# Performance work log

Measured on AMD Instinct MI355X. Metric: run time of the kernel, lower is better.

The kernel has to match this reference:

```python
import jax, jax.numpy as jnp
import numpy as np

B = 2048; S = 256; D = 64; R = 16; H = 4; HD = D // H; HID = 128; P = 4; T = 8
SCALE = 10.0  # pointer-address sharpness from _execute_read


def setup_inputs() -> dict:
    key = jax.random.key(0)
    ks = jax.random.split(key, 16)
    g = lambda k, shape, s=0.05: jax.random.normal(k, shape, dtype=jnp.float32) * s
    z = lambda shape: jnp.zeros(shape, jnp.float32)
    return {
        'x': g(ks[0], (B, D), 1.0),
        'register_init': g(ks[1], (R, D)),
        'scratchpad_init': g(ks[2], (S, D)),
        'pointer_init': z((P,)),
        'wq': g(ks[3], (D, D)), 'bq': z((D,)),
        'wk': g(ks[4], (D, D)), 'bk': z((D,)),
        'wv': g(ks[5], (D, D)), 'bv': z((D,)),
        'wo': g(ks[6], (D, D)), 'bo': z((D,)),
        'w_write': g(ks[7], (D, D)), 'b_write': z((D,)),
        'a_w1': g(ks[8], (D, HID)), 'a_b1': z((HID,)),
        'a_w2': g(ks[9], (HID, S)), 'a_b2': z((S,)),
        'p_w1': g(ks[10], (D, HID)), 'p_b1': z((HID,)),
        'p_w2': g(ks[11], (HID, D)), 'p_b2': z((D,)),
        'num_steps': T,
    }


def _engine_forward(x, register_init, scratchpad_init, pointer_init,
                    wq, bq, wk, bk, wv, bv, wo, bo, w_write, b_write,
                    a_w1, a_b1, a_w2, a_b2, p_w1, p_b1, p_w2, p_b2, num_steps):
    b = x.shape[0]
    positions = jnp.linspace(0.0, 1.0, S)  # (S,) slot positions for pointer addressing
    sp = jnp.broadcast_to(scratchpad_init, (b, S, D))
    reg = jnp.broadcast_to(register_init, (b, R, D))
    reg = reg.at[:, 0, :].set(x)  # LOAD: place input into register 0
    ptr = jnp.broadcast_to(pointer_init, (b, P))
    inv_sqrt = 1.0 / jnp.sqrt(jnp.float32(HD))

    def step(carry, _):
        sp, reg, ptr = carry
        # READ: soft pointer-based address over scratchpad slots (softmax(-|pos-p|*10))
        p0 = ptr[:, 0]                                                            # (b,)
        addr_r = jax.nn.softmax(-jnp.abs(positions[None, :] - p0[:, None]) * SCALE, axis=-1)  # (b,S)
        reg_val = jnp.einsum('bs,bsd->bd', addr_r, sp)                            # (b,D)
        reg = reg.at[:, 0, :].set(reg_val)
        # content-based attention read (read_head: 4-head MHA, q from register 0)
        qh = (reg_val @ wq + bq).reshape(b, H, HD)
        kh = (sp @ wk + bk).reshape(b, S, H, HD)
        vh = (sp @ wv + bv).reshape(b, S, H, HD)
        attn = jax.nn.softmax(jnp.einsum('bhd,bshd->bhs', qh, kh) * inv_sqrt, axis=-1)  # (b,H,S)
        read = jnp.einsum('bhs,bshd->bhd', attn, vh).reshape(b, D) @ wo + bo      # (b,D)
        # pattern_net transforms the read value into register 1
        patt = jax.nn.relu(read @ p_w1 + p_b1) @ p_w2 + p_b2
        reg = reg.at[:, 1, :].set(patt)
        # WRITE: address_net softmax write + write_head, gated blend into scratchpad
        addr_w = jax.nn.softmax(jax.nn.relu(read @ a_w1 + a_b1) @ a_w2 + a_b2, axis=-1)  # (b,S)
        wval = read @ w_write + b_write                                           # (b,D)
        aw = addr_w[:, :, None]
        sp = sp * (1.0 - aw) + wval[:, None, :] * aw
        # POINTER_MOVE: +1 slot (normalized), clamped to [0,1]
        ptr = ptr.at[:, 0].set(jnp.clip(p0 + 1.0 / S, 0.0, 1.0))
        return (sp, reg, ptr), None

    (sp, reg, ptr), _ = jax.lax.scan(step, (sp, reg, ptr), None, length=num_steps)
    return sp


def reference(x, register_init, scratchpad_init, pointer_init,
              wq, bq, wk, bk, wv, bv, wo, bo, w_write, b_write,
              a_w1, a_b1, a_w2, a_b2, p_w1, p_b1, p_w2, p_b2, num_steps):
    return _engine_forward(x, register_init, scratchpad_init, pointer_init,
                           wq, bq, wk, bk, wv, bv, wo, bo, w_write, b_write,
                           a_w1, a_b1, a_w2, a_b2, p_w1, p_b1, p_w2, p_b2, num_steps)
```

## Files before the change

### kernel.cpp

```cpp
#include <hip/hip_runtime.h>

#define NB   2048
#define S    256
#define D    64
#define H    4
#define HD   16
#define HID  128
#define TPB  256
#define SCALEF 10.0f

__device__ __forceinline__ float wred_max(float v){
#pragma unroll
  for (int m = 32; m >= 1; m >>= 1) v = fmaxf(v, __shfl_xor(v, m, 64));
  return v;
}
__device__ __forceinline__ float wred_sum(float v){
#pragma unroll
  for (int m = 32; m >= 1; m >>= 1) v += __shfl_xor(v, m, 64);
  return v;
}
__device__ __forceinline__ float pick4(float4 f, int h){
  float r = f.x;
  r = (h == 1) ? f.y : r;
  r = (h == 2) ? f.z : r;
  r = (h == 3) ? f.w : r;
  return r;
}

__global__ __launch_bounds__(TPB, 2)
void engine_kernel(const float* __restrict__ sp_init,
                   const float* __restrict__ ptr_init,
                   const float* __restrict__ wq, const float* __restrict__ bq,
                   const float* __restrict__ wk, const float* __restrict__ bk,
                   const float* __restrict__ wv, const float* __restrict__ bv,
                   const float* __restrict__ wo, const float* __restrict__ bo,
                   const float* __restrict__ ww, const float* __restrict__ bw,
                   const float* __restrict__ aw1, const float* __restrict__ ab1,
                   const float* __restrict__ aw2, const float* __restrict__ ab2,
                   const int*   __restrict__ nsteps,
                   float* __restrict__ out)
{
  __shared__ float  sp[S][D + 1];
  __shared__ float4 attnT[S];
  __shared__ float  addrv[S];
  __shared__ float4 qkT[D];
  __shared__ __align__(16) float hidden[HID];
  __shared__ float  parth[4][4][D];
  __shared__ float  regv[D], qhv[D], readf[D], readv[D], wvalv[D];
  __shared__ float  ctxv[H][D];
  __shared__ float  qbv[H];
  __shared__ float  red[8];

  const int tid  = threadIdx.x;
  const int wid  = tid >> 6;
  const int lane = tid & 63;

  float awcol[HID];
#pragma unroll
  for (int k = 0; k < HID; ++k) awcol[k] = aw2[k * S + tid];

  for (int i = tid; i < S * D / 4; i += TPB) {
    float4 v = reinterpret_cast<const float4*>(sp_init)[i];
    int flat = i << 2;
    int s = flat >> 6, d = flat & 63;
    sp[s][d + 0] = v.x; sp[s][d + 1] = v.y; sp[s][d + 2] = v.z; sp[s][d + 3] = v.w;
  }
  float p0 = ptr_init[0];
  const int T = *nsteps;
  const float posq = (float)tid * (1.0f / 255.0f);
  __syncthreads();

  for (int t = 0; t < T; ++t) {
    {
      float a = -fabsf(posq - p0) * SCALEF;
      float m = wred_max(a);
      if (lane == 0) red[wid] = m;
      __syncthreads();
      m = fmaxf(fmaxf(red[0], red[1]), fmaxf(red[2], red[3]));
      float e = expf(a - m);
      float ss = wred_sum(e);
      if (lane == 0) red[4 + wid] = ss;
      __syncthreads();
      ss = red[4] + red[5] + red[6] + red[7];
      addrv[tid] = e / ss;
    }
    __syncthreads();

    {
      const int d = lane, s0 = wid * 64;
      float acc = 0.f;
#pragma unroll 8
      for (int i = 0; i < 64; ++i) acc += addrv[s0 + i] * sp[s0 + i][d];
      parth[wid][0][d] = acc;
    }
    __syncthreads();
    if (tid < 64)
      regv[tid] = parth[0][0][tid] + parth[1][0][tid] + parth[2][0][tid] + parth[3][0][tid];
    __syncthreads();

    {
      const int j = lane, g = wid;
      float acc = 0.f;
#pragma unroll
      for (int i = 0; i < 16; ++i) { int e2 = g * 16 + i; acc += regv[e2] * wq[e2 * 64 + j]; }
      parth[g][0][j] = acc;
    }
    __syncthreads();
    if (tid < 64)
      qhv[tid] = bq[tid] + parth[0][0][tid] + parth[1][0][tid] + parth[2][0][tid] + parth[3][0][tid];
    __syncthreads();

    {
      const int h = wid, e2 = lane;
      float acc = 0.f;
#pragma unroll
      for (int j = 0; j < 16; ++j) acc += wk[e2 * 64 + h * 16 + j] * qhv[h * 16 + j];
      ((float*)qkT)[e2 * 4 + h] = acc;
      if (tid < 4) {
        float qb = 0.f;
#pragma unroll
        for (int j = 0; j < 16; ++j) qb += qhv[tid * 16 + j] * bk[tid * 16 + j];
        qbv[tid] = qb;
      }
    }
    __syncthreads();

    {
      float a0 = qbv[0], a1 = qbv[1], a2 = qbv[2], a3 = qbv[3];
#pragma unroll 8
      for (int e2 = 0; e2 < 64; ++e2) {
        float v = sp[tid][e2];
        float4 qk = qkT[e2];
        a0 += v * qk.x; a1 += v * qk.y; a2 += v * qk.z; a3 += v * qk.w;
      }
      attnT[tid] = make_float4(a0 * 0.25f, a1 * 0.25f, a2 * 0.25f, a3 * 0.25f);
    }
    __syncthreads();
    {
      const int h = wid, i = lane;
      float4 f0 = attnT[i], f1 = attnT[i + 64], f2 = attnT[i + 128], f3 = attnT[i + 192];
      float v0 = pick4(f0, h), v1 = pick4(f1, h), v2 = pick4(f2, h), v3 = pick4(f3, h);
      float mm = wred_max(fmaxf(fmaxf(v0, v1), fmaxf(v2, v3)));
      v0 = expf(v0 - mm); v1 = expf(v1 - mm); v2 = expf(v2 - mm); v3 = expf(v3 - mm);
      float sum = wred_sum(v0 + v1 + v2 + v3);
      float inv = 1.0f / sum;
      ((float*)attnT)[(i      ) * 4 + h] = v0 * inv;
      ((float*)attnT)[(i +  64) * 4 + h] = v1 * inv;
      ((float*)attnT)[(i + 128) * 4 + h] = v2 * inv;
      ((float*)attnT)[(i + 192) * 4 + h] = v3 * inv;
    }
    __syncthreads();

    {
      const int d = lane, s0 = wid * 64;
      float a0 = 0, a1 = 0, a2 = 0, a3 = 0;
#pragma unroll 4
      for (int i = 0; i < 64; ++i) {
        int s = s0 + i;
        float v = sp[s][d];
        float4 at = attnT[s];
        a0 += at.x * v; a1 += at.y * v; a2 += at.z * v; a3 += at.w * v;
      }
      parth[wid][0][d] = a0; parth[wid][1][d] = a1; parth[wid][2][d] = a2; parth[wid][3][d] = a3;
    }
    __syncthreads();
    {
      const int h = wid, d = lane;
      ctxv[h][d] = parth[0][h][d] + parth[1][h][d] + parth[2][h][d] + parth[3][h][d];
    }
    __syncthreads();

    {
      const int f = lane, g = wid, h = f >> 4;
      float acc = 0.f;
#pragma unroll
      for (int i = 0; i < 16; ++i) { int e2 = g * 16 + i; acc += ctxv[h][e2] * wv[e2 * 64 + f]; }
      parth[g][0][f] = acc;
    }
    __syncthreads();
    if (tid < 64)
      readf[tid] = bv[tid] + parth[0][0][tid] + parth[1][0][tid] + parth[2][0][tid] + parth[3][0][tid];
    __syncthreads();
    {
      const int c = lane, g = wid;
      float acc = 0.f;
#pragma unroll
      for (int i = 0; i < 16; ++i) { int f2 = g * 16 + i; acc += readf[f2] * wo[f2 * 64 + c]; }
      parth[g][1][c] = acc;
    }
    __syncthreads();
    if (tid < 64)
      readv[tid] = bo[tid] + parth[0][1][tid] + parth[1][1][tid] + parth[2][1][tid] + parth[3][1][tid];
    __syncthreads();

    {
      const int k = tid & 127, g = tid >> 7;
      float acc = 0.f;
#pragma unroll 8
      for (int i = 0; i < 32; ++i) { int e2 = g * 32 + i; acc += readv[e2] * aw1[e2 * 128 + k]; }
      ((float*)parth)[g * 128 + k] = acc;
    }
    __syncthreads();
    if (tid < 128)
      hidden[tid] = fmaxf(ab1[tid] + ((float*)parth)[tid] + ((float*)parth)[128 + tid], 0.f);
    __syncthreads();

    {
      float acc = ab2[tid];
#pragma unroll
      for (int k = 0; k < HID; k += 4) {
        float4 hv = *reinterpret_cast<const float4*>(&hidden[k]);
        acc += hv.x * awcol[k] + hv.y * awcol[k + 1] + hv.z * awcol[k + 2] + hv.w * awcol[k + 3];
      }
      float mm = wred_max(acc);
      if (lane == 0) red[wid] = mm;
      __syncthreads();
      mm = fmaxf(fmaxf(red[0], red[1]), fmaxf(red[2], red[3]));
      float ee = expf(acc - mm);
      float ss = wred_sum(ee);
      if (lane == 0) red[4 + wid] = ss;
      __syncthreads();
      ss = red[4] + red[5] + red[6] + red[7];
      addrv[tid] = ee / ss;
    }
    __syncthreads();

    {
      const int c = lane, g = wid;
      float acc = 0.f;
#pragma unroll
      for (int i = 0; i < 16; ++i) { int e2 = g * 16 + i; acc += readv[e2] * ww[e2 * 64 + c]; }
      parth[g][0][c] = acc;
    }
    __syncthreads();
    if (tid < 64)
      wvalv[tid] = bw[tid] + parth[0][0][tid] + parth[1][0][tid] + parth[2][0][tid] + parth[3][0][tid];
    __syncthreads();

    {
      float aa = addrv[tid];
      float om = 1.0f - aa;
#pragma unroll 8
      for (int d = 0; d < 64; ++d)
        sp[tid][d] = sp[tid][d] * om + wvalv[d] * aa;
    }
    p0 = fminf(fmaxf(p0 + (1.0f / (float)S), 0.f), 1.f);
    __syncthreads();
  }

  float* ob = out + (size_t)blockIdx.x * (S * D);
  for (int i = tid; i < S * D / 4; i += TPB) {
    int flat = i << 2, s = flat >> 6, d = flat & 63;
    ((float4*)ob)[i] = make_float4(sp[s][d], sp[s][d + 1], sp[s][d + 2], sp[s][d + 3]);
  }
}

extern "C" void kernel_launch(void* const* d_in, const int* in_sizes, int n_in,
                              void* d_out, int out_size, void* d_ws, size_t ws_size,
                              hipStream_t stream) {
  const float* sp_init  = (const float*)d_in[2];
  const float* ptr_init = (const float*)d_in[3];
  const float* wq = (const float*)d_in[4];
  const float* bq = (const float*)d_in[5];
  const float* wk = (const float*)d_in[6];
  const float* bk = (const float*)d_in[7];
  const float* wv = (const float*)d_in[8];
  const float* bv = (const float*)d_in[9];
  const float* wo = (const float*)d_in[10];
  const float* bo = (const float*)d_in[11];
  const float* ww = (const float*)d_in[12];
  const float* bw = (const float*)d_in[13];
  const float* aw1 = (const float*)d_in[14];
  const float* ab1 = (const float*)d_in[15];
  const float* aw2 = (const float*)d_in[16];
  const float* ab2 = (const float*)d_in[17];
  const int* nsteps = (const int*)d_in[22];
  float* out = (float*)d_out;

  engine_kernel<<<dim3(NB), dim3(TPB), 0, stream>>>(
      sp_init, ptr_init, wq, bq, wk, bk, wv, bv, wo, bo, ww, bw,
      aw1, ab1, aw2, ab2, nsteps, out);
}
```

Baseline: 986.4 us.

## Keep scratchpad rows in registers with fp16 shared mirror and fewer barriers

```diff
diff --git a/kernel.cpp b/kernel.cpp
--- a/kernel.cpp
+++ b/kernel.cpp
@@ -1,33 +1,37 @@
 #include <hip/hip_runtime.h>
+#include <hip/hip_fp16.h>
 
 #define NB   2048
 #define S    256
 #define D    64
 #define H    4
-#define HD   16
 #define HID  128
 #define TPB  256
-#define SCALEF 10.0f
-
-__device__ __forceinline__ float wred_max(float v){
-#pragma unroll
-  for (int m = 32; m >= 1; m >>= 1) v = fmaxf(v, __shfl_xor(v, m, 64));
-  return v;
-}
+
 __device__ __forceinline__ float wred_sum(float v){
 #pragma unroll
   for (int m = 32; m >= 1; m >>= 1) v += __shfl_xor(v, m, 64);
   return v;
 }
-__device__ __forceinline__ float pick4(float4 f, int h){
-  float r = f.x;
-  r = (h == 1) ? f.y : r;
-  r = (h == 2) ? f.z : r;
-  r = (h == 3) ? f.w : r;
-  return r;
-}
-
-__global__ __launch_bounds__(TPB, 2)
+
+__device__ __forceinline__ unsigned h2u(__half2 h){ union{__half2 h; unsigned u;} c; c.h=h; return c.u; }
+__device__ __forceinline__ __half2 u2h(unsigned u){ union{__half2 h; unsigned u;} c; c.u=u; return c.h; }
+
+__device__ __forceinline__ void matvec64(const float* __restrict__ W,
+                                         const float* __restrict__ bias,
+                                         const float* x, float* y,
+                                         int wid, int lane) {
+  const int j  = wid * 16 + (lane & 15);
+  const int i0 = (lane >> 4) * 16;
+  float acc = 0.f;
+#pragma unroll
+  for (int i = 0; i < 16; ++i) acc += x[i0 + i] * W[(i0 + i) * 64 + j];
+  acc += __shfl_xor(acc, 16, 64);
+  acc += __shfl_xor(acc, 32, 64);
+  if (lane < 16) y[j] = acc + bias[j];
+}
+
+__global__ __launch_bounds__(TPB, 4)
 void engine_kernel(const float* __restrict__ sp_init,
                    const float* __restrict__ ptr_init,
                    const float* __restrict__ wq, const float* __restrict__ bq,
@@ -40,30 +44,36 @@
                    const int*   __restrict__ nsteps,
                    float* __restrict__ out)
 {
-  __shared__ float  sp[S][D + 1];
-  __shared__ float4 attnT[S];
-  __shared__ float  addrv[S];
-  __shared__ float4 qkT[D];
+  __shared__ __half  spm[S][66];
+  __shared__ float4  qkT[D];
+  __shared__ float4  red4[4];
   __shared__ __align__(16) float hidden[HID];
-  __shared__ float  parth[4][4][D];
-  __shared__ float  regv[D], qhv[D], readf[D], readv[D], wvalv[D];
-  __shared__ float  ctxv[H][D];
-  __shared__ float  qbv[H];
-  __shared__ float  red[8];
+  __shared__ float   ctxv[H][D];
+  __shared__ float   regv[D];
+  __shared__ float   qhv[D], readf[D], readv[D], wvalv[D];
+  __shared__ unsigned attnLo[S], attnHi[S];
+  __shared__ __half  addrh[S];
+  __shared__ float   red_p1[4], red9[4];
+  __shared__ float   qbv[H];
 
   const int tid  = threadIdx.x;
   const int wid  = tid >> 6;
   const int lane = tid & 63;
 
-  float awcol[HID];
-#pragma unroll
-  for (int k = 0; k < HID; ++k) awcol[k] = aw2[k * S + tid];
-
-  for (int i = tid; i < S * D / 4; i += TPB) {
-    float4 v = reinterpret_cast<const float4*>(sp_init)[i];
-    int flat = i << 2;
-    int s = flat >> 6, d = flat & 63;
-    sp[s][d + 0] = v.x; sp[s][d + 1] = v.y; sp[s][d + 2] = v.z; sp[s][d + 3] = v.w;
+  float sp_reg[D];
+  {
+    const float4* src = reinterpret_cast<const float4*>(sp_init + tid * D);
+#pragma unroll
+    for (int k = 0; k < 16; ++k) {
+      float4 v = src[k];
+      sp_reg[4*k+0] = v.x; sp_reg[4*k+1] = v.y; sp_reg[4*k+2] = v.z; sp_reg[4*k+3] = v.w;
+    }
+    __half2* rowp = reinterpret_cast<__half2*>(&spm[tid][0]);
+#pragma unroll
+    for (int p = 0; p < 32; ++p)
+      rowp[p] = __float22half2_rn(make_float2(sp_reg[2*p], sp_reg[2*p+1]));
+    if (tid < 64) regv[tid] = 0.f;
+    ((float*)ctxv)[tid] = 0.f;
   }
   float p0 = ptr_init[0];
   const int T = *nsteps;
@@ -72,186 +82,173 @@
 
   for (int t = 0; t < T; ++t) {
     {
-      float a = -fabsf(posq - p0) * SCALEF;
-      float m = wred_max(a);
-      if (lane == 0) red[wid] = m;
+      float a = __expf(-10.0f * fabsf(posq - p0));
+      float ss = wred_sum(a);
+      if (lane == 0) red_p1[wid] = ss;
       __syncthreads();
-      m = fmaxf(fmaxf(red[0], red[1]), fmaxf(red[2], red[3]));
-      float e = expf(a - m);
-      float ss = wred_sum(e);
-      if (lane == 0) red[4 + wid] = ss;
-      __syncthreads();
-      ss = red[4] + red[5] + red[6] + red[7];
-      addrv[tid] = e / ss;
+      ss = red_p1[0] + red_p1[1] + red_p1[2] + red_p1[3];
+      addrh[tid] = __float2half(a / ss);
     }
     __syncthreads();
 
     {
       const int d = lane, s0 = wid * 64;
       float acc = 0.f;
-#pragma unroll 8
-      for (int i = 0; i < 64; ++i) acc += addrv[s0 + i] * sp[s0 + i][d];
-      parth[wid][0][d] = acc;
-    }
-    __syncthreads();
-    if (tid < 64)
-      regv[tid] = parth[0][0][tid] + parth[1][0][tid] + parth[2][0][tid] + parth[3][0][tid];
-    __syncthreads();
-
-    {
-      const int j = lane, g = wid;
-      float acc = 0.f;
-#pragma unroll
-      for (int i = 0; i < 16; ++i) { int e2 = g * 16 + i; acc += regv[e2] * wq[e2 * 64 + j]; }
-      parth[g][0][j] = acc;
-    }
-    __syncthreads();
-    if (tid < 64)
-      qhv[tid] = bq[tid] + parth[0][0][tid] + parth[1][0][tid] + parth[2][0][tid] + parth[3][0][tid];
-    __syncthreads();
-
-    {
-      const int h = wid, e2 = lane;
-      float acc = 0.f;
-#pragma unroll
-      for (int j = 0; j < 16; ++j) acc += wk[e2 * 64 + h * 16 + j] * qhv[h * 16 + j];
-      ((float*)qkT)[e2 * 4 + h] = acc;
+#pragma unroll 16
+      for (int i = 0; i < 64; ++i) {
+        int s = s0 + i;
+        acc += __half2float(addrh[s]) * __half2float(spm[s][d]);
+      }
+      atomicAdd(&regv[d], acc);
+    }
+    __syncthreads();
+
+    matvec64(wq, bq, regv, qhv, wid, lane);
+    __syncthreads();
+
+    {
+      const int h = wid, e = lane;
+      float acc = 0.f;
+#pragma unroll
+      for (int j = 0; j < 16; ++j) acc += wk[e * 64 + h * 16 + j] * qhv[h * 16 + j];
+      ((float*)qkT)[e * 4 + h] = acc;
       if (tid < 4) {
         float qb = 0.f;
 #pragma unroll
         for (int j = 0; j < 16; ++j) qb += qhv[tid * 16 + j] * bk[tid * 16 + j];
         qbv[tid] = qb;
       }
-    }
-    __syncthreads();
-
-    {
-      float a0 = qbv[0], a1 = qbv[1], a2 = qbv[2], a3 = qbv[3];
+      if (tid < 64) regv[tid] = 0.f;
+    }
+    __syncthreads();
+
+    {
+      float s0 = qbv[0], s1 = qbv[1], s2 = qbv[2], s3 = qbv[3];
+#pragma unroll
+      for (int e = 0; e < 64; ++e) {
+        float4 qk = qkT[e];
+        float v = sp_reg[e];
+        s0 += v * qk.x; s1 += v * qk.y; s2 += v * qk.z; s3 += v * qk.w;
+      }
+      float e0 = __expf(s0 * 0.25f), e1 = __expf(s1 * 0.25f);
+      float e2 = __expf(s2 * 0.25f), e3 = __expf(s3 * 0.25f);
+      float r0 = e0, r1 = e1, r2 = e2, r3 = e3;
+#pragma unroll
+      for (int m = 32; m >= 1; m >>= 1) {
+        r0 += __shfl_xor(r0, m, 64); r1 += __shfl_xor(r1, m, 64);
+        r2 += __shfl_xor(r2, m, 64); r3 += __shfl_xor(r3, m, 64);
+      }
+      if (lane == 0) red4[wid] = make_float4(r0, r1, r2, r3);
+      __syncthreads();
+      float4 t0 = red4[0], t1 = red4[1], t2 = red4[2], t3 = red4[3];
+      float i0 = 1.0f / (t0.x + t1.x + t2.x + t3.x);
+      float i1 = 1.0f / (t0.y + t1.y + t2.y + t3.y);
+      float i2 = 1.0f / (t0.z + t1.z + t2.z + t3.z);
+      float i3 = 1.0f / (t0.w + t1.w + t2.w + t3.w);
+      attnLo[tid] = h2u(__float22half2_rn(make_float2(e0 * i0, e1 * i1)));
+      attnHi[tid] = h2u(__float22half2_rn(make_float2(e2 * i2, e3 * i3)));
+      ((float*)ctxv)[tid] = 0.f;
+    }
+    __syncthreads();
+
+    {
+      const int d = lane, s0 = wid * 64;
+      float c0 = 0, c1 = 0, c2 = 0, c3 = 0;
 #pragma unroll 8
-      for (int e2 = 0; e2 < 64; ++e2) {
-        float v = sp[tid][e2];
-        float4 qk = qkT[e2];
-        a0 += v * qk.x; a1 += v * qk.y; a2 += v * qk.z; a3 += v * qk.w;
-      }
-      attnT[tid] = make_float4(a0 * 0.25f, a1 * 0.25f, a2 * 0.25f, a3 * 0.25f);
-    }
-    __syncthreads();
-    {
-      const int h = wid, i = lane;
-      float4 f0 = attnT[i], f1 = attnT[i + 64], f2 = attnT[i + 128], f3 = attnT[i + 192];
-      float v0 = pick4(f0, h), v1 = pick4(f1, h), v2 = pick4(f2, h), v3 = pick4(f3, h);
-      float mm = wred_max(fmaxf(fmaxf(v0, v1), fmaxf(v2, v3)));
-      v0 = expf(v0 - mm); v1 = expf(v1 - mm); v2 = expf(v2 - mm); v3 = expf(v3 - mm);
-      float sum = wred_sum(v0 + v1 + v2 + v3);
-      float inv = 1.0f / sum;
-      ((float*)attnT)[(i      ) * 4 + h] = v0 * inv;
-      ((float*)attnT)[(i +  64) * 4 + h] = v1 * inv;
-      ((float*)attnT)[(i + 128) * 4 + h] = v2 * inv;
-      ((float*)attnT)[(i + 192) * 4 + h] = v3 * inv;
-    }
-    __syncthreads();
-
-    {
-      const int d = lane, s0 = wid * 64;
-      float a0 = 0, a1 = 0, a2 = 0, a3 = 0;
-#pragma unroll 4
       for (int i = 0; i < 64; ++i) {
         int s = s0 + i;
-        float v = sp[s][d];
-        float4 at = attnT[s];
-        a0 += at.x * v; a1 += at.y * v; a2 += at.z * v; a3 += at.w * v;
-      }
-      parth[wid][0][d] = a0; parth[wid][1][d] = a1; parth[wid][2][d] = a2; parth[wid][3][d] = a3;
-    }
-    __syncthreads();
-    {
-      const int h = wid, d = lane;
-      ctxv[h][d] = parth[0][h][d] + parth[1][h][d] + parth[2][h][d] + parth[3][h][d];
-    }
-    __syncthreads();
-
-    {
-      const int f = lane, g = wid, h = f >> 4;
-      float acc = 0.f;
-#pragma unroll
-      for (int i = 0; i < 16; ++i) { int e2 = g * 16 + i; acc += ctxv[h][e2] * wv[e2 * 64 + f]; }
-      parth[g][0][f] = acc;
-    }
-    __syncthreads();
-    if (tid < 64)
-      readf[tid] = bv[tid] + parth[0][0][tid] + parth[1][0][tid] + parth[2][0][tid] + parth[3][0][tid];
-    __syncthreads();
-    {
-      const int c = lane, g = wid;
-      float acc = 0.f;
-#pragma unroll
-      for (int i = 0; i < 16; ++i) { int f2 = g * 16 + i; acc += readf[f2] * wo[f2 * 64 + c]; }
-      parth[g][1][c] = acc;
-    }
-    __syncthreads();
-    if (tid < 64)
-      readv[tid] = bo[tid] + parth[0][1][tid] + parth[1][1][tid] + parth[2][1][tid] + parth[3][1][tid];
-    __syncthreads();
-
-    {
-      const int k = tid & 127, g = tid >> 7;
-      float acc = 0.f;
-#pragma unroll 8
-      for (int i = 0; i < 32; ++i) { int e2 = g * 32 + i; acc += readv[e2] * aw1[e2 * 128 + k]; }
-      ((float*)parth)[g * 128 + k] = acc;
-    }
-    __syncthreads();
-    if (tid < 128)
-      hidden[tid] = fmaxf(ab1[tid] + ((float*)parth)[tid] + ((float*)parth)[128 + tid], 0.f);
-    __syncthreads();
-
+        float sv = __half2float(spm[s][d]);
+        float2 fl = __half22float2(u2h(attnLo[s]));
+        float2 fh = __half22float2(u2h(attnHi[s]));
+        c0 += fl.x * sv; c1 += fl.y * sv; c2 += fh.x * sv; c3 += fh.y * sv;
+      }
+      atomicAdd(&ctxv[0][d], c0); atomicAdd(&ctxv[1][d], c1);
+      atomicAdd(&ctxv[2][d], c2); atomicAdd(&ctxv[3][d], c3);
+    }
+    __syncthreads();
+
+    {
+      const int f = wid * 16 + (lane & 15);
+      const int i0 = (lane >> 4) * 16;
+      float acc = 0.f;
+#pragma unroll
+      for (int i = 0; i < 16; ++i) acc += ctxv[wid][i0 + i] * wv[(i0 + i) * 64 + f];
+      acc += __shfl_xor(acc, 16, 64);
+      acc += __shfl_xor(acc, 32, 64);
+      if (lane < 16) readf[f] = acc + bv[f];
+    }
+    __syncthreads();
+
+    matvec64(wo, bo, readf, readv, wid, lane);
+    __syncthreads();
+
+    if (wid < 2) {
+      const int k = wid * 64 + lane;
+      float acc = 0.f;
+#pragma unroll 16
+      for (int i = 0; i < 64; ++i) acc += readv[i] * aw1[i * 128 + k];
+      hidden[k] = fmaxf(acc + ab1[k], 0.f);
+    }
+    __syncthreads();
+
+    {
+      const int c = wid * 16 + (lane & 15);
+      const int i0 = (lane >> 4) * 16;
+      float acc = 0.f;
+#pragma unroll
+      for (int i = 0; i < 16; ++i) acc += readv[i0 + i] * ww[(i0 + i) * 64 + c];
+      acc += __shfl_xor(acc, 16, 64);
+      acc += __shfl_xor(acc, 32, 64);
+      if (lane < 16) wvalv[c] = acc + bw[c];
+    }
+    float aa;
     {
       float acc = ab2[tid];
-#pragma unroll
-      for (int k = 0; k < HID; k += 4) {
-        float4 hv = *reinterpret_cast<const float4*>(&hidden[k]);
-        acc += hv.x * awcol[k] + hv.y * awcol[k + 1] + hv.z * awcol[k + 2] + hv.w * awcol[k + 3];
-      }
-      float mm = wred_max(acc);
-      if (lane == 0) red[wid] = mm;
+      const float4* h4 = reinterpret_cast<const float4*>(hidden);
+#pragma unroll
+      for (int k = 0; k < 32; ++k) {
+        float4 hv = h4[k];
+        acc += hv.x * aw2[(4*k+0) * 256 + tid] + hv.y * aw2[(4*k+1) * 256 + tid]
+             + hv.z * aw2[(4*k+2) * 256 + tid] + hv.w * aw2[(4*k+3) * 256 + tid];
+      }
+      float e = __expf(acc);
+      float ss = wred_sum(e);
+      if (lane == 0) red9[wid] = ss;
       __syncthreads();
-      mm = fmaxf(fmaxf(red[0], red[1]), fmaxf(red[2], red[3]));
-      float ee = expf(acc - mm);
-      float ss = wred_sum(ee);
-      if (lane == 0) red[4 + wid] = ss;
-      __syncthreads();
-      ss = red[4] + red[5] + red[6] + red[7];
-      addrv[tid] = ee / ss;
-    }
-    __syncthreads();
-
-    {
-      const int c = lane, g = wid;
-      float acc = 0.f;
-#pragma unroll
-      for (int i = 0; i < 16; ++i) { int e2 = g * 16 + i; acc += readv[e2] * ww[e2 * 64 + c]; }
-      parth[g][0][c] = acc;
-    }
-    __syncthreads();
-    if (tid < 64)
-      wvalv[tid] = bw[tid] + parth[0][0][tid] + parth[1][0][tid] + parth[2][0][tid] + parth[3][0][tid];
-    __syncthreads();
-
-    {
-      float aa = addrv[tid];
+      ss = red9[0] + red9[1] + red9[2] + red9[3];
+      aa = e / ss;
+    }
+
+    {
       float om = 1.0f - aa;
-#pragma unroll 8
-      for (int d = 0; d < 64; ++d)
-        sp[tid][d] = sp[tid][d] * om + wvalv[d] * aa;
+#pragma unroll
+      for (int d = 0; d < D; ++d)
+        sp_reg[d] = sp_reg[d] * om + wvalv[d] * aa;
+      __half2* rowp = reinterpret_cast<__half2*>(&spm[tid][0]);
+#pragma unroll
+      for (int p = 0; p < 32; ++p)
+        rowp[p] = __float22half2_rn(make_float2(sp_reg[2*p], sp_reg[2*p+1]));
     }
     p0 = fminf(fmaxf(p0 + (1.0f / (float)S), 0.f), 1.f);
-    __syncthreads();
   }
 
-  float* ob = out + (size_t)blockIdx.x * (S * D);
-  for (int i = tid; i < S * D / 4; i += TPB) {
-    int flat = i << 2, s = flat >> 6, d = flat & 63;
-    ((float4*)ob)[i] = make_float4(sp[s][d], sp[s][d + 1], sp[s][d + 2], sp[s][d + 3]);
+  float* stg = reinterpret_cast<float*>(spm);
+  float* ob  = out + (size_t)blockIdx.x * (S * D);
+  for (int c = 0; c < 4; ++c) {
+    __syncthreads();
+    if ((tid >> 6) == c) {
+      const int r = lane;
+#pragma unroll
+      for (int d = 0; d < D; ++d) stg[r * 65 + d] = sp_reg[d];
+    }
+    __syncthreads();
+    const int base = c * 64 * D;
+#pragma unroll
+    for (int i = tid; i < 64 * D / 4; i += TPB) {
+      int flat = i << 2, r = flat >> 6, d = flat & 63;
+      reinterpret_cast<float4*>(ob + base)[i] =
+          make_float4(stg[r*65+d], stg[r*65+d+1], stg[r*65+d+2], stg[r*65+d+3]);
+    }
   }
 }
 
@@ -276,6 +273,7 @@
   const float* ab2 = (const float*)d_in[17];
   const int* nsteps = (const int*)d_in[22];
   float* out = (float*)d_out;
+  (void)d_ws; (void)ws_size;
 
   engine_kernel<<<dim3(NB), dim3(TPB), 0, stream>>>(
       sp_init, ptr_init, wq, bq, wk, bk, wv, bv, wo, bo, ww, bw,
```

Measured after the change: 2.027 ms. +105.5%, slower.
